# Kernel tuning notes

Hardware: AMD Instinct MI355X
Metric: run time of the kernel (lower is better)

Reference implementation:

```python
import jax, jax.numpy as jnp
import numpy as np

B, S, H, NH, L = 2, 2048, 2048, 16, 512
HD = H // NH  # head_dim = 128


def setup_inputs() -> dict:
    key = jax.random.key(0)
    k1, k2, k3, k4, k5 = jax.random.split(key, 5)
    scale = 0.02  # mimic xavier-scale init
    return {
        "q": jax.random.normal(k1, (B, S, H), dtype=jnp.float32),
        "latent_kv": jax.random.normal(k2, (B, S, L), dtype=jnp.float32),
        "Wq": jax.random.normal(k3, (H, H), dtype=jnp.float32) * scale,
        "Wkv_expand": jax.random.normal(k4, (2 * H, L), dtype=jnp.float32) * scale,
        "Wout": jax.random.normal(k5, (H, H), dtype=jnp.float32) * scale,
    }


def reference(q, latent_kv, Wq, Wkv_expand, Wout):
    b, sq, _ = q.shape
    sk = latent_kv.shape[1]
    # projections (torch Linear: x @ W.T)
    qp = q @ Wq.T                              # [B,Sq,H]
    kv = latent_kv @ Wkv_expand.T              # [B,Sk,2H]
    k, v = jnp.split(kv, 2, axis=-1)           # each [B,Sk,H]
    # split heads -> [B,NH,S,HD]
    qh = qp.reshape(b, sq, NH, HD).transpose(0, 2, 1, 3)
    kh = k.reshape(b, sk, NH, HD).transpose(0, 2, 1, 3)
    vh = v.reshape(b, sk, NH, HD).transpose(0, 2, 1, 3)
    inv_sqrt_d = 1.0 / jnp.sqrt(jnp.float32(HD))
    scores = jnp.einsum("bhqd,bhkd->bhqk", qh, kh) * inv_sqrt_d
    # causal mask (seq_q == seq_k)
    causal = jnp.tril(jnp.ones((sq, sk), dtype=bool))
    scores = jnp.where(causal, scores, jnp.finfo(scores.dtype).min)
    attn = jax.nn.softmax(scores, axis=-1)
    out = jnp.einsum("bhqk,bhkd->bhqd", attn, vh)  # [B,NH,Sq,HD]
    out = out.transpose(0, 2, 1, 3).reshape(b, sq, H)
    return out @ Wout.T
```

## Files before the change

### kernel.cpp

```cpp
#include <hip/hip_runtime.h>

#define SLEN 2048
#define NHEADS 16
#define HDIM 128

typedef __attribute__((ext_vector_type(8))) short bf16x8;
typedef __attribute__((ext_vector_type(4))) float f32x4;
typedef __attribute__((ext_vector_type(16))) float f32x16;

__device__ __forceinline__ unsigned short f2bf(float f) {
  union { float f; unsigned u; } v; v.f = f;
  unsigned r = v.u + 0x7FFFu + ((v.u >> 16) & 1u);
  return (unsigned short)(r >> 16);
}

__device__ __forceinline__ float bf2f(unsigned short h) {
  union { unsigned u; float f; } v; v.u = (unsigned)h << 16;
  return v.f;
}

__device__ __forceinline__ unsigned pkbf(float a, float b) {
  unsigned r;
  asm("v_cvt_pk_bf16_f32 %0, %1, %2" : "=v"(r) : "v"(a), "v"(b));
  return r;
}

__device__ __forceinline__ void gload16(const void* g, void* l) {
  __builtin_amdgcn_global_load_lds(
      (const __attribute__((address_space(1))) unsigned int*)g,
      (__attribute__((address_space(3))) unsigned int*)l, 16, 0, 0);
}

__global__ __launch_bounds__(256) void cvt_all(const float* __restrict__ q,
                                               const float* __restrict__ Wq,
                                               const float* __restrict__ lat,
                                               const float* __restrict__ Wkv,
                                               const float* __restrict__ Wout,
                                               unsigned short* __restrict__ qo,
                                               unsigned short* __restrict__ Wqo,
                                               unsigned short* __restrict__ lato,
                                               unsigned short* __restrict__ Wkvo,
                                               unsigned short* __restrict__ Wouto) {
  const int blk = blockIdx.x;
  const float* in;
  unsigned short* out;
  int base;
  if (blk < 4096)      { in = q;    out = qo;    base = 0; }
  else if (blk < 6144) { in = Wq;   out = Wqo;   base = 4096; }
  else if (blk < 7168) { in = lat;  out = lato;  base = 6144; }
  else if (blk < 8192) { in = Wkv;  out = Wkvo;  base = 7168; }
  else                 { in = Wout; out = Wouto; base = 8192; }
  const int i = (blk - base) * 256 + threadIdx.x;
  const float4* p = reinterpret_cast<const float4*>(in) + (size_t)i * 2;
  float4 a = p[0], b = p[1];
  uint4 o;
  o.x = (unsigned)f2bf(a.x) | ((unsigned)f2bf(a.y) << 16);
  o.y = (unsigned)f2bf(a.z) | ((unsigned)f2bf(a.w) << 16);
  o.z = (unsigned)f2bf(b.x) | ((unsigned)f2bf(b.y) << 16);
  o.w = (unsigned)f2bf(b.z) | ((unsigned)f2bf(b.w) << 16);
  reinterpret_cast<uint4*>(out)[i] = o;
}

template <bool OUT_F32>
__global__ __launch_bounds__(256) void gemm_bt(const unsigned short* __restrict__ A,
                                               const unsigned short* __restrict__ B,
                                               void* __restrict__ Cv,
                                               int M, int N, int K) {
  __shared__ unsigned short As[128 * 32];
  __shared__ unsigned short Bs[128 * 32];
  const int tid = threadIdx.x;
  const int lane = tid & 63, wid = tid >> 6;
  const int g = lane >> 4, q = lane & 15;
  const int nbx = N >> 7;
  const int bx = blockIdx.x % nbx, by = blockIdx.x / nbx;
  const int tM = by << 7, tN = bx << 7;
  const int wm = (wid >> 1) * 64, wn = (wid & 1) * 64;

  f32x4 acc[4][4] = {};

  const int o0 = tid * 16;
  const int r0 = o0 >> 6, c0 = (o0 & 63) >> 1;
  const int r1 = r0 + 64;
  const unsigned short* gA0 = A + (size_t)(tM + r0) * K + c0;
  const unsigned short* gA1 = A + (size_t)(tM + r1) * K + c0;
  const unsigned short* gB0 = B + (size_t)(tN + r0) * K + c0;
  const unsigned short* gB1 = B + (size_t)(tN + r1) * K + c0;
  char* lA = (char*)As;
  char* lB = (char*)Bs;
  const int wo = wid * 1024;

  for (int kt = 0; kt < K; kt += 32) {
    gload16(gA0, lA + wo);
    gload16(gA1, lA + 4096 + wo);
    gload16(gB0, lB + wo);
    gload16(gB1, lB + 4096 + wo);
    gA0 += 32; gA1 += 32; gB0 += 32; gB1 += 32;
    __syncthreads();
    bf16x8 af[4], bfr[4];
#pragma unroll
    for (int i = 0; i < 4; ++i)
      af[i] = *(const bf16x8*)&As[(wm + i * 16 + q) * 32 + g * 8];
#pragma unroll
    for (int j = 0; j < 4; ++j)
      bfr[j] = *(const bf16x8*)&Bs[(wn + j * 16 + q) * 32 + g * 8];
#pragma unroll
    for (int i = 0; i < 4; ++i)
#pragma unroll
      for (int j = 0; j < 4; ++j)
        acc[i][j] = __builtin_amdgcn_mfma_f32_16x16x32_bf16(af[i], bfr[j], acc[i][j], 0, 0, 0);
    __syncthreads();
  }

  if constexpr (OUT_F32) {
    float* C = (float*)Cv;
#pragma unroll
    for (int i = 0; i < 4; ++i)
#pragma unroll
      for (int j = 0; j < 4; ++j)
#pragma unroll
        for (int r = 0; r < 4; ++r)
          C[(size_t)(tM + wm + i * 16 + g * 4 + r) * N + (tN + wn + j * 16 + q)] =
              acc[i][j][r];
  } else {
    unsigned short* C = (unsigned short*)Cv;
#pragma unroll
    for (int i = 0; i < 4; ++i)
#pragma unroll
      for (int j = 0; j < 4; ++j)
#pragma unroll
        for (int r = 0; r < 4; ++r)
          C[(size_t)(tM + wm + i * 16 + g * 4 + r) * N + (tN + wn + j * 16 + q)] =
              f2bf(acc[i][j][r]);
  }
}

__global__ __launch_bounds__(256, 2) void mla_attn(const unsigned short* __restrict__ Q,
                                                   const unsigned short* __restrict__ K,
                                                   const unsigned short* __restrict__ VT,
                                                   unsigned short* __restrict__ Opart,
                                                   float* __restrict__ Stats) {
  __shared__ unsigned short Ks[2][64 * 128];
  __shared__ unsigned short Vs[2][128 * 64];

  const int tid = threadIdx.x, lane = tid & 63, w = tid >> 6;
  const int q5 = lane & 31, half = lane >> 5, q7 = lane & 7;
  const int s = blockIdx.x & 1;
  const int pr = (blockIdx.x >> 1) & 7;
  const int bh = blockIdx.x >> 4;
  const int head = bh & 15, b = bh >> 4;

  const unsigned short* Kbase = K + (size_t)(b * 2048) * 2048 + head * 128;
  const unsigned short* Vbase = VT + (size_t)(b * 2048 + head * 128) * 2048;

  const int r0 = tid >> 4, c0 = tid & 15;
  const unsigned short* kS = Kbase + (size_t)r0 * 2048 + ((c0 ^ r0) << 3);
  const int d0 = tid >> 3, c3 = tid & 7;
  const unsigned short* vS = Vbase + (size_t)d0 * 2048 + ((c3 ^ (d0 & 7)) << 3);

  const float sc_f = 0.08838834764831845f;
  const int arow0 = q5 * 256;
  const int vrow0 = q5 * 128;
  const int q15 = q5 & 15;

  for (int t2 = 0; t2 < 2; ++t2) {
    const int qt = t2 ? pr : 15 - pr;
    const int kt0 = s * (qt + 1);
    const int ktN = kt0 + qt + 1;
    const int myq = qt * 128 + w * 32 + q5;
    const unsigned short* Qrow = Q + (size_t)(b * 2048 + myq) * 2048 + head * 128;

    bf16x8 qf[8];
#pragma unroll
    for (int ks = 0; ks < 8; ++ks)
      qf[ks] = *(const bf16x8*)((const char*)Qrow + ks * 32 + half * 16);

    __syncthreads();

    {
      const int kvb0 = kt0 * 64;
      unsigned short* kd = &Ks[kt0 & 1][0] + tid * 8;
      unsigned short* vd = &Vs[kt0 & 1][0] + tid * 8;
      const unsigned short* ks2 = kS + (size_t)kvb0 * 2048;
      const unsigned short* vs2 = vS + kvb0;
#pragma unroll
      for (int u = 0; u < 4; ++u) {
        gload16(ks2 + (size_t)u * 16 * 2048, kd + u * 2048);
        gload16(vs2 + (size_t)u * 32 * 2048, vd + u * 2048);
      }
    }

    float m2 = -1e30f, l = 0.f;
    f32x16 o[4];
#pragma unroll
    for (int i = 0; i < 16; ++i) { o[0][i] = 0.f; o[1][i] = 0.f; o[2][i] = 0.f; o[3][i] = 0.f; }

    for (int kt = kt0; kt < ktN; ++kt) {
      const int cur = kt & 1;
      asm volatile("s_waitcnt vmcnt(0)" ::: "memory");
      __builtin_amdgcn_s_barrier();

      if (kt + 1 < ktN) {
        const int kvb2 = (kt + 1) * 64;
        unsigned short* kd = &Ks[cur ^ 1][0] + tid * 8;
        unsigned short* vd = &Vs[cur ^ 1][0] + tid * 8;
        const unsigned short* ks2 = kS + (size_t)kvb2 * 2048;
        const unsigned short* vs2 = vS + kvb2;
#pragma unroll
        for (int u = 0; u < 4; ++u) {
          gload16(ks2 + (size_t)u * 16 * 2048, kd + u * 2048);
          gload16(vs2 + (size_t)u * 32 * 2048, vd + u * 2048);
        }
      }

      f32x16 st[2];
#pragma unroll
      for (int i = 0; i < 16; ++i) { st[0][i] = 0.f; st[1][i] = 0.f; }
      const char* kb = (const char*)&Ks[cur][0];
      __builtin_amdgcn_s_setprio(1);
#pragma unroll
      for (int ks = 0; ks < 8; ++ks) {
        const int cd = ks * 2 + half;
#pragma unroll
        for (int m = 0; m < 2; ++m) {
          bf16x8 kf = *(const bf16x8*)(kb + arow0 + m * 8192 + ((cd ^ q15) << 4));
          st[m] = __builtin_amdgcn_mfma_f32_32x32x16_bf16(kf, qf[ks], st[m], 0, 0, 0);
        }
      }
      __builtin_amdgcn_s_setprio(0);

      float t[32];
      const int kvb = kt * 64;
      const bool needmask = (kvb + 63 > qt * 128 + w * 32);
#pragma unroll
      for (int m = 0; m < 2; ++m)
#pragma unroll
        for (int r = 0; r < 16; ++r) {
          float sv = st[m][r] * sc_f;
          if (needmask) {
            const int kvloc = m * 32 + (r & 3) + 8 * (r >> 2) + 4 * half;
            sv = (kvb + kvloc <= myq) ? sv : -3e38f;
          }
          t[m * 16 + r] = sv;
        }
      float mx = t[0];
#pragma unroll
      for (int i = 1; i < 32; ++i) mx = fmaxf(mx, t[i]);
      mx = fmaxf(mx, __shfl_xor(mx, 32));

      if (!__all(mx <= m2 + 8.f)) {
        const float mnew = fmaxf(m2, mx);
        const float rsc = __expf(m2 - mnew);
        m2 = mnew; l *= rsc;
#pragma unroll
        for (int r = 0; r < 16; ++r) {
          const int rowv = (r & 3) + 8 * (r >> 2) + 4 * half;
          const float f = __shfl(rsc, rowv);
          o[0][r] *= f; o[1][r] *= f; o[2][r] *= f; o[3][r] *= f;
        }
      }

      float ts = 0.f;
#pragma unroll
      for (int i = 0; i < 32; ++i) { t[i] = __expf(t[i] - m2); ts += t[i]; }
      ts += __shfl_xor(ts, 32);
      l += ts;

      unsigned wpk[2][4][2];
#pragma unroll
      for (int m = 0; m < 2; ++m)
#pragma unroll
        for (int r4 = 0; r4 < 4; ++r4) {
          wpk[m][r4][0] = pkbf(t[m * 16 + r4 * 4 + 0], t[m * 16 + r4 * 4 + 1]);
          wpk[m][r4][1] = pkbf(t[m * 16 + r4 * 4 + 2], t[m * 16 + r4 * 4 + 3]);
        }

      const char* vb = (const char*)&Vs[cur][0];
#pragma unroll
      for (int ks = 0; ks < 4; ++ks) {
        const int m = ks >> 1, i = ks & 1;
        const unsigned s0 = half ? wpk[m][2 * i][0] : wpk[m][2 * i + 1][0];
        const unsigned s1 = half ? wpk[m][2 * i][1] : wpk[m][2 * i + 1][1];
        const unsigned rv0 = (unsigned)__shfl_xor((int)s0, 32);
        const unsigned rv1 = (unsigned)__shfl_xor((int)s1, 32);
        const unsigned ow0 = half ? wpk[m][2 * i + 1][0] : wpk[m][2 * i][0];
        const unsigned ow1 = half ? wpk[m][2 * i + 1][1] : wpk[m][2 * i][1];
        union { unsigned u[4]; bf16x8 v; } fr;
        fr.u[0] = half ? rv0 : ow0;
        fr.u[1] = half ? rv1 : ow1;
        fr.u[2] = half ? ow0 : rv0;
        fr.u[3] = half ? ow1 : rv1;
        const int cd = ks * 2 + half;
        __builtin_amdgcn_s_setprio(1);
#pragma unroll
        for (int nf = 0; nf < 4; ++nf) {
          bf16x8 vf = *(const bf16x8*)(vb + vrow0 + nf * 4096 + ((cd ^ q7) << 4));
          o[nf] = __builtin_amdgcn_mfma_f32_32x32x16_bf16(fr.v, vf, o[nf], 0, 0, 0);
        }
        __builtin_amdgcn_s_setprio(0);
      }
    }

    const int base_o = ((bh * 16 + qt) * 2 + s) << 14;
    const int base_s = ((bh * 16 + qt) * 2 + s) << 8;
    if (half == 0) {
      Stats[base_s + (w * 32 + q5) * 2] = m2;
      Stats[base_s + (w * 32 + q5) * 2 + 1] = l;
    }
#pragma unroll
    for (int r = 0; r < 16; ++r) {
      const int rowv = (r & 3) + 8 * (r >> 2) + 4 * half;
      const int row = w * 32 + rowv;
#pragma unroll
      for (int nf = 0; nf < 4; ++nf)
        Opart[base_o + row * 128 + nf * 32 + q5] = f2bf(o[nf][r]);
    }
  }
}

__global__ __launch_bounds__(256) void mla_merge(const unsigned short* __restrict__ Op,
                                                 const float* __restrict__ St,
                                                 unsigned short* __restrict__ AO) {
  const int idx = blockIdx.x * 256 + threadIdx.x;
  const int rid = idx >> 4;
  const int d0 = (idx & 15) << 3;
  const int bhqt = rid >> 7;
  const int row = rid & 127;
  const int sb = bhqt << 1;
  const float m1 = St[(sb << 8) + row * 2];
  const float l1 = St[(sb << 8) + row * 2 + 1];
  const float m2 = St[(sb << 8) + 256 + row * 2];
  const float l2 = St[(sb << 8) + 256 + row * 2 + 1];
  const float M = fmaxf(m1, m2);
  const float w1 = __expf(m1 - M), w2 = __expf(m2 - M);
  const float inv = 1.0f / (w1 * l1 + w2 * l2);
  const unsigned short* p1 = Op + ((size_t)sb << 14) + row * 128 + d0;
  bf16x8 a = *(const bf16x8*)p1;
  bf16x8 c = *(const bf16x8*)(p1 + 16384);
  const int bh = bhqt >> 4, qt = bhqt & 15;
  const int head = bh & 15, b = bh >> 4;
  unsigned short outv[8];
#pragma unroll
  for (int j = 0; j < 8; ++j)
    outv[j] = f2bf((w1 * bf2f((unsigned short)a[j]) + w2 * bf2f((unsigned short)c[j])) * inv);
  unsigned short* dst = AO + ((size_t)(b * 2048 + qt * 128 + row)) * 2048 + head * 128 + d0;
  *(uint4*)dst = *(const uint4*)outv;
}

extern "C" void kernel_launch(void* const* d_in, const int* in_sizes, int n_in,
                              void* d_out, int out_size, void* d_ws, size_t ws_size,
                              hipStream_t stream) {
  const float* q    = (const float*)d_in[0];
  const float* lat  = (const float*)d_in[1];
  const float* Wq   = (const float*)d_in[2];
  const float* Wkv  = (const float*)d_in[3];
  const float* Wout = (const float*)d_in[4];

  char* ws = (char*)d_ws;
  unsigned short* qbf   = (unsigned short*)(ws);
  unsigned short* Opart = (unsigned short*)(ws);
  unsigned short* Wqbf  = (unsigned short*)(ws + 16777216);
  unsigned short* latbf = (unsigned short*)(ws + 25165824);
  unsigned short* Wkvbf = (unsigned short*)(ws + 29360128);
  unsigned short* Wobf  = (unsigned short*)(ws + 33554432);
  unsigned short* qpbf  = (unsigned short*)(ws + 41943040);
  unsigned short* Kbf   = (unsigned short*)(ws + 58720256);
  unsigned short* aobf  = (unsigned short*)(ws + 58720256);
  unsigned short* VTbf  = (unsigned short*)(ws + 75497472);
  float*          Stats = (float*)(ws + 92274688);
  unsigned short* Wvbf  = Wkvbf + (size_t)2048 * 512;

  cvt_all<<<10240, 256, 0, stream>>>(q, Wq, lat, Wkv, Wout,
                                     qbf, Wqbf, latbf, Wkvbf, Wobf);

  gemm_bt<false><<<512, 256, 0, stream>>>(qbf, Wqbf, qpbf, 4096, 2048, 2048);
  gemm_bt<false><<<512, 256, 0, stream>>>(latbf, Wkvbf, Kbf, 4096, 2048, 512);
  gemm_bt<false><<<256, 256, 0, stream>>>(Wvbf, latbf, VTbf, 2048, 2048, 512);
  gemm_bt<false><<<256, 256, 0, stream>>>(Wvbf, latbf + (size_t)2048 * 512,
                                          VTbf + (size_t)2048 * 2048, 2048, 2048, 512);
  mla_attn<<<512, 256, 0, stream>>>(qpbf, Kbf, VTbf, Opart, Stats);
  mla_merge<<<4096, 256, 0, stream>>>(Opart, Stats, aobf);
  gemm_bt<true><<<512, 256, 0, stream>>>(aobf, Wobf, (float*)d_out, 4096, 2048, 2048);
}
```

Baseline: 246.7 us.

## Enlarge attention query tile to 256 rows with 8 waves and triple-buffered KV

The attention kernel now runs 512-thread blocks covering 256 query rows, so each K/V tile loaded into shared memory is reused by twice as many waves. K/V staging moves from double to triple buffering with a two-tile prefetch distance and a partial vmcnt wait, so loads overlap more compute. The two V-transpose GEMM launches are merged into one launch using a z-grid batch offset. Costs are higher LDS use (one block per CU) and half as many attention blocks, which may reduce occupancy and worsen causal load balance.

```diff
diff --git a/kernel.cpp b/kernel.cpp
--- a/kernel.cpp
+++ b/kernel.cpp
@@ -65,7 +65,8 @@
 __global__ __launch_bounds__(256) void gemm_bt(const unsigned short* __restrict__ A,
                                                const unsigned short* __restrict__ B,
                                                void* __restrict__ Cv,
-                                               int M, int N, int K) {
+                                               int M, int N, int K,
+                                               size_t zB, size_t zC) {
   __shared__ unsigned short As[128 * 32];
   __shared__ unsigned short Bs[128 * 32];
   const int tid = threadIdx.x;
@@ -75,6 +76,8 @@
   const int bx = blockIdx.x % nbx, by = blockIdx.x / nbx;
   const int tM = by << 7, tN = bx << 7;
   const int wm = (wid >> 1) * 64, wn = (wid & 1) * 64;
+  const size_t zoff = (size_t)blockIdx.z;
+  B += zoff * zB;
 
   f32x4 acc[4][4] = {};
 
@@ -112,7 +115,7 @@
   }
 
   if constexpr (OUT_F32) {
-    float* C = (float*)Cv;
+    float* C = (float*)Cv + zoff * zC;
 #pragma unroll
     for (int i = 0; i < 4; ++i)
 #pragma unroll
@@ -122,7 +125,7 @@
           C[(size_t)(tM + wm + i * 16 + g * 4 + r) * N + (tN + wn + j * 16 + q)] =
               acc[i][j][r];
   } else {
-    unsigned short* C = (unsigned short*)Cv;
+    unsigned short* C = (unsigned short*)Cv + zoff * zC;
 #pragma unroll
     for (int i = 0; i < 4; ++i)
 #pragma unroll
@@ -134,26 +137,26 @@
   }
 }
 
-__global__ __launch_bounds__(256, 2) void mla_attn(const unsigned short* __restrict__ Q,
+__global__ __launch_bounds__(512, 1) void mla_attn(const unsigned short* __restrict__ Q,
                                                    const unsigned short* __restrict__ K,
                                                    const unsigned short* __restrict__ VT,
                                                    unsigned short* __restrict__ Opart,
                                                    float* __restrict__ Stats) {
-  __shared__ unsigned short Ks[2][64 * 128];
-  __shared__ unsigned short Vs[2][128 * 64];
+  __shared__ unsigned short Ks[3][64 * 128];
+  __shared__ unsigned short Vs[3][128 * 64];
 
   const int tid = threadIdx.x, lane = tid & 63, w = tid >> 6;
   const int q5 = lane & 31, half = lane >> 5, q7 = lane & 7;
   const int s = blockIdx.x & 1;
-  const int pr = (blockIdx.x >> 1) & 7;
-  const int bh = blockIdx.x >> 4;
+  const int pr = (blockIdx.x >> 1) & 3;
+  const int bh = blockIdx.x >> 3;
   const int head = bh & 15, b = bh >> 4;
 
   const unsigned short* Kbase = K + (size_t)(b * 2048) * 2048 + head * 128;
   const unsigned short* Vbase = VT + (size_t)(b * 2048 + head * 128) * 2048;
 
   const int r0 = tid >> 4, c0 = tid & 15;
-  const unsigned short* kS = Kbase + (size_t)r0 * 2048 + ((c0 ^ r0) << 3);
+  const unsigned short* kS = Kbase + (size_t)r0 * 2048 + ((c0 ^ (r0 & 15)) << 3);
   const int d0 = tid >> 3, c3 = tid & 7;
   const unsigned short* vS = Vbase + (size_t)d0 * 2048 + ((c3 ^ (d0 & 7)) << 3);
 
@@ -163,10 +166,10 @@
   const int q15 = q5 & 15;
 
   for (int t2 = 0; t2 < 2; ++t2) {
-    const int qt = t2 ? pr : 15 - pr;
-    const int kt0 = s * (qt + 1);
-    const int ktN = kt0 + qt + 1;
-    const int myq = qt * 128 + w * 32 + q5;
+    const int qt = t2 ? pr : 7 - pr;
+    const int kt0 = s * 2 * (qt + 1);
+    const int ktN = kt0 + 2 * (qt + 1);
+    const int myq = qt * 256 + w * 32 + q5;
     const unsigned short* Qrow = Q + (size_t)(b * 2048 + myq) * 2048 + head * 128;
 
     bf16x8 qf[8];
@@ -176,17 +179,26 @@
 
     __syncthreads();
 
+    int cur = kt0 % 3;
     {
+      const int n1 = cur + 1 == 3 ? 0 : cur + 1;
       const int kvb0 = kt0 * 64;
-      unsigned short* kd = &Ks[kt0 & 1][0] + tid * 8;
-      unsigned short* vd = &Vs[kt0 & 1][0] + tid * 8;
+      unsigned short* kd = &Ks[cur][0] + tid * 8;
+      unsigned short* vd = &Vs[cur][0] + tid * 8;
       const unsigned short* ks2 = kS + (size_t)kvb0 * 2048;
       const unsigned short* vs2 = vS + kvb0;
-#pragma unroll
-      for (int u = 0; u < 4; ++u) {
-        gload16(ks2 + (size_t)u * 16 * 2048, kd + u * 2048);
-        gload16(vs2 + (size_t)u * 32 * 2048, vd + u * 2048);
-      }
+      gload16(ks2, kd);
+      gload16(ks2 + (size_t)32 * 2048, kd + 4096);
+      gload16(vs2, vd);
+      gload16(vs2 + (size_t)64 * 2048, vd + 4096);
+      unsigned short* kd1 = &Ks[n1][0] + tid * 8;
+      unsigned short* vd1 = &Vs[n1][0] + tid * 8;
+      const unsigned short* ks3 = ks2 + (size_t)64 * 2048;
+      const unsigned short* vs3 = vs2 + 64;
+      gload16(ks3, kd1);
+      gload16(ks3 + (size_t)32 * 2048, kd1 + 4096);
+      gload16(vs3, vd1);
+      gload16(vs3 + (size_t)64 * 2048, vd1 + 4096);
     }
 
     float m2 = -1e30f, l = 0.f;
@@ -195,21 +207,21 @@
     for (int i = 0; i < 16; ++i) { o[0][i] = 0.f; o[1][i] = 0.f; o[2][i] = 0.f; o[3][i] = 0.f; }
 
     for (int kt = kt0; kt < ktN; ++kt) {
-      const int cur = kt & 1;
-      asm volatile("s_waitcnt vmcnt(0)" ::: "memory");
+      if (kt + 1 < ktN) asm volatile("s_waitcnt vmcnt(4)" ::: "memory");
+      else              asm volatile("s_waitcnt vmcnt(0)" ::: "memory");
       __builtin_amdgcn_s_barrier();
 
-      if (kt + 1 < ktN) {
-        const int kvb2 = (kt + 1) * 64;
-        unsigned short* kd = &Ks[cur ^ 1][0] + tid * 8;
-        unsigned short* vd = &Vs[cur ^ 1][0] + tid * 8;
+      if (kt + 2 < ktN) {
+        const int n2 = cur >= 1 ? cur - 1 : cur + 2;
+        const int kvb2 = (kt + 2) * 64;
+        unsigned short* kd = &Ks[n2][0] + tid * 8;
+        unsigned short* vd = &Vs[n2][0] + tid * 8;
         const unsigned short* ks2 = kS + (size_t)kvb2 * 2048;
         const unsigned short* vs2 = vS + kvb2;
-#pragma unroll
-        for (int u = 0; u < 4; ++u) {
-          gload16(ks2 + (size_t)u * 16 * 2048, kd + u * 2048);
-          gload16(vs2 + (size_t)u * 32 * 2048, vd + u * 2048);
-        }
+        gload16(ks2, kd);
+        gload16(ks2 + (size_t)32 * 2048, kd + 4096);
+        gload16(vs2, vd);
+        gload16(vs2 + (size_t)64 * 2048, vd + 4096);
       }
 
       f32x16 st[2];
@@ -230,7 +242,7 @@
 
       float t[32];
       const int kvb = kt * 64;
-      const bool needmask = (kvb + 63 > qt * 128 + w * 32);
+      const bool needmask = (kvb + 63 > qt * 256 + w * 32);
 #pragma unroll
       for (int m = 0; m < 2; ++m)
 #pragma unroll
@@ -298,10 +310,13 @@
         }
         __builtin_amdgcn_s_setprio(0);
       }
+
+      cur = cur + 1 == 3 ? 0 : cur + 1;
     }
 
-    const int base_o = ((bh * 16 + qt) * 2 + s) << 14;
-    const int base_s = ((bh * 16 + qt) * 2 + s) << 8;
+    const int set = (bh * 8 + qt) * 2 + s;
+    const int base_o = set << 15;
+    const int base_s = set << 9;
     if (half == 0) {
       Stats[base_s + (w * 32 + q5) * 2] = m2;
       Stats[base_s + (w * 32 + q5) * 2 + 1] = l;
@@ -323,26 +338,26 @@
   const int idx = blockIdx.x * 256 + threadIdx.x;
   const int rid = idx >> 4;
   const int d0 = (idx & 15) << 3;
-  const int bhqt = rid >> 7;
-  const int row = rid & 127;
+  const int bhqt = rid >> 8;
+  const int row = rid & 255;
   const int sb = bhqt << 1;
-  const float m1 = St[(sb << 8) + row * 2];
-  const float l1 = St[(sb << 8) + row * 2 + 1];
-  const float m2 = St[(sb << 8) + 256 + row * 2];
-  const float l2 = St[(sb << 8) + 256 + row * 2 + 1];
+  const float m1 = St[(sb << 9) + row * 2];
+  const float l1 = St[(sb << 9) + row * 2 + 1];
+  const float m2 = St[((sb + 1) << 9) + row * 2];
+  const float l2 = St[((sb + 1) << 9) + row * 2 + 1];
   const float M = fmaxf(m1, m2);
   const float w1 = __expf(m1 - M), w2 = __expf(m2 - M);
   const float inv = 1.0f / (w1 * l1 + w2 * l2);
-  const unsigned short* p1 = Op + ((size_t)sb << 14) + row * 128 + d0;
+  const unsigned short* p1 = Op + ((size_t)sb << 15) + row * 128 + d0;
   bf16x8 a = *(const bf16x8*)p1;
-  bf16x8 c = *(const bf16x8*)(p1 + 16384);
-  const int bh = bhqt >> 4, qt = bhqt & 15;
+  bf16x8 c = *(const bf16x8*)(p1 + 32768);
+  const int bh = bhqt >> 3, qt = bhqt & 7;
   const int head = bh & 15, b = bh >> 4;
   unsigned short outv[8];
 #pragma unroll
   for (int j = 0; j < 8; ++j)
     outv[j] = f2bf((w1 * bf2f((unsigned short)a[j]) + w2 * bf2f((unsigned short)c[j])) * inv);
-  unsigned short* dst = AO + ((size_t)(b * 2048 + qt * 128 + row)) * 2048 + head * 128 + d0;
+  unsigned short* dst = AO + ((size_t)(b * 2048 + qt * 256 + row)) * 2048 + head * 128 + d0;
   *(uint4*)dst = *(const uint4*)outv;
 }
 
@@ -372,12 +387,12 @@
   cvt_all<<<10240, 256, 0, stream>>>(q, Wq, lat, Wkv, Wout,
                                      qbf, Wqbf, latbf, Wkvbf, Wobf);
 
-  gemm_bt<false><<<512, 256, 0, stream>>>(qbf, Wqbf, qpbf, 4096, 2048, 2048);
-  gemm_bt<false><<<512, 256, 0, stream>>>(latbf, Wkvbf, Kbf, 4096, 2048, 512);
-  gemm_bt<false><<<256, 256, 0, stream>>>(Wvbf, latbf, VTbf, 2048, 2048, 512);
-  gemm_bt<false><<<256, 256, 0, stream>>>(Wvbf, latbf + (size_t)2048 * 512,
-                                          VTbf + (size_t)2048 * 2048, 2048, 2048, 512);
-  mla_attn<<<512, 256, 0, stream>>>(qpbf, Kbf, VTbf, Opart, Stats);
+  gemm_bt<false><<<512, 256, 0, stream>>>(qbf, Wqbf, qpbf, 4096, 2048, 2048, 0, 0);
+  gemm_bt<false><<<512, 256, 0, stream>>>(latbf, Wkvbf, Kbf, 4096, 2048, 512, 0, 0);
+  gemm_bt<false><<<dim3(256, 1, 2), 256, 0, stream>>>(
+      Wvbf, latbf, VTbf, 2048, 2048, 512,
+      (size_t)2048 * 512, (size_t)2048 * 2048);
+  mla_attn<<<256, 512, 0, stream>>>(qpbf, Kbf, VTbf, Opart, Stats);
   mla_merge<<<4096, 256, 0, stream>>>(Opart, Stats, aobf);
-  gemm_bt<true><<<512, 256, 0, stream>>>(aobf, Wobf, (float*)d_out, 4096, 2048, 2048);
-}
+  gemm_bt<true><<<512, 256, 0, stream>>>(aobf, Wobf, (float*)d_out, 4096, 2048, 2048, 0, 0);
+}
```

Result: faster. 240.7 us (-2.4%).

## Fold softmax scale into Q projection, split K/V waits, batch V GEMMs

Applied to the files above, without the earlier changes.

Multiplies the Q projection output by 1/sqrt(d)·log2(e) so the attention loop drops its per-score multiply and uses exp2 directly. The merge kernel and the skip-rescale threshold are adjusted to match the base-2 domain. K loads are issued before V loads, and a partial vmcnt wait plus a second barrier let the V tile keep arriving while the QK^T and softmax work runs. The two V-transpose GEMM launches are merged into one launch with a z-dimension. Storing pre-scaled Q in bf16 slightly changes rounding, and the extra barrier adds some synchronisation cost.

```diff
diff --git a/kernel.cpp b/kernel.cpp
--- a/kernel.cpp
+++ b/kernel.cpp
@@ -65,7 +65,8 @@
 __global__ __launch_bounds__(256) void gemm_bt(const unsigned short* __restrict__ A,
                                                const unsigned short* __restrict__ B,
                                                void* __restrict__ Cv,
-                                               int M, int N, int K) {
+                                               int M, int N, int K,
+                                               size_t zB, size_t zC, float scale) {
   __shared__ unsigned short As[128 * 32];
   __shared__ unsigned short Bs[128 * 32];
   const int tid = threadIdx.x;
@@ -75,6 +76,8 @@
   const int bx = blockIdx.x % nbx, by = blockIdx.x / nbx;
   const int tM = by << 7, tN = bx << 7;
   const int wm = (wid >> 1) * 64, wn = (wid & 1) * 64;
+  const size_t zoff = (size_t)blockIdx.z;
+  B += zoff * zB;
 
   f32x4 acc[4][4] = {};
 
@@ -112,7 +115,7 @@
   }
 
   if constexpr (OUT_F32) {
-    float* C = (float*)Cv;
+    float* C = (float*)Cv + zoff * zC;
 #pragma unroll
     for (int i = 0; i < 4; ++i)
 #pragma unroll
@@ -120,9 +123,9 @@
 #pragma unroll
         for (int r = 0; r < 4; ++r)
           C[(size_t)(tM + wm + i * 16 + g * 4 + r) * N + (tN + wn + j * 16 + q)] =
-              acc[i][j][r];
+              acc[i][j][r] * scale;
   } else {
-    unsigned short* C = (unsigned short*)Cv;
+    unsigned short* C = (unsigned short*)Cv + zoff * zC;
 #pragma unroll
     for (int i = 0; i < 4; ++i)
 #pragma unroll
@@ -130,7 +133,7 @@
 #pragma unroll
         for (int r = 0; r < 4; ++r)
           C[(size_t)(tM + wm + i * 16 + g * 4 + r) * N + (tN + wn + j * 16 + q)] =
-              f2bf(acc[i][j][r]);
+              f2bf(acc[i][j][r] * scale);
   }
 }
 
@@ -157,7 +160,6 @@
   const int d0 = tid >> 3, c3 = tid & 7;
   const unsigned short* vS = Vbase + (size_t)d0 * 2048 + ((c3 ^ (d0 & 7)) << 3);
 
-  const float sc_f = 0.08838834764831845f;
   const int arow0 = q5 * 256;
   const int vrow0 = q5 * 128;
   const int q15 = q5 & 15;
@@ -183,10 +185,9 @@
       const unsigned short* ks2 = kS + (size_t)kvb0 * 2048;
       const unsigned short* vs2 = vS + kvb0;
 #pragma unroll
-      for (int u = 0; u < 4; ++u) {
-        gload16(ks2 + (size_t)u * 16 * 2048, kd + u * 2048);
-        gload16(vs2 + (size_t)u * 32 * 2048, vd + u * 2048);
-      }
+      for (int u = 0; u < 4; ++u) gload16(ks2 + (size_t)u * 16 * 2048, kd + u * 2048);
+#pragma unroll
+      for (int u = 0; u < 4; ++u) gload16(vs2 + (size_t)u * 32 * 2048, vd + u * 2048);
     }
 
     float m2 = -1e30f, l = 0.f;
@@ -196,7 +197,7 @@
 
     for (int kt = kt0; kt < ktN; ++kt) {
       const int cur = kt & 1;
-      asm volatile("s_waitcnt vmcnt(0)" ::: "memory");
+      asm volatile("s_waitcnt vmcnt(4)" ::: "memory");
       __builtin_amdgcn_s_barrier();
 
       if (kt + 1 < ktN) {
@@ -206,10 +207,9 @@
         const unsigned short* ks2 = kS + (size_t)kvb2 * 2048;
         const unsigned short* vs2 = vS + kvb2;
 #pragma unroll
-        for (int u = 0; u < 4; ++u) {
-          gload16(ks2 + (size_t)u * 16 * 2048, kd + u * 2048);
-          gload16(vs2 + (size_t)u * 32 * 2048, vd + u * 2048);
-        }
+        for (int u = 0; u < 4; ++u) gload16(ks2 + (size_t)u * 16 * 2048, kd + u * 2048);
+#pragma unroll
+        for (int u = 0; u < 4; ++u) gload16(vs2 + (size_t)u * 32 * 2048, vd + u * 2048);
       }
 
       f32x16 st[2];
@@ -235,21 +235,21 @@
       for (int m = 0; m < 2; ++m)
 #pragma unroll
         for (int r = 0; r < 16; ++r) {
-          float sv = st[m][r] * sc_f;
+          float sv = st[m][r];
           if (needmask) {
             const int kvloc = m * 32 + (r & 3) + 8 * (r >> 2) + 4 * half;
             sv = (kvb + kvloc <= myq) ? sv : -3e38f;
           }
           t[m * 16 + r] = sv;
         }
-      float mx = t[0];
-#pragma unroll
-      for (int i = 1; i < 32; ++i) mx = fmaxf(mx, t[i]);
+      float mx = fmaxf(t[0], t[1]);
+#pragma unroll
+      for (int i = 2; i < 32; i += 2) mx = fmaxf(fmaxf(mx, t[i]), t[i + 1]);
       mx = fmaxf(mx, __shfl_xor(mx, 32));
 
-      if (!__all(mx <= m2 + 8.f)) {
+      if (!__all(mx <= m2 + 11.54f)) {
         const float mnew = fmaxf(m2, mx);
-        const float rsc = __expf(m2 - mnew);
+        const float rsc = __builtin_amdgcn_exp2f(m2 - mnew);
         m2 = mnew; l *= rsc;
 #pragma unroll
         for (int r = 0; r < 16; ++r) {
@@ -261,7 +261,7 @@
 
       float ts = 0.f;
 #pragma unroll
-      for (int i = 0; i < 32; ++i) { t[i] = __expf(t[i] - m2); ts += t[i]; }
+      for (int i = 0; i < 32; ++i) { t[i] = __builtin_amdgcn_exp2f(t[i] - m2); ts += t[i]; }
       ts += __shfl_xor(ts, 32);
       l += ts;
 
@@ -273,6 +273,10 @@
           wpk[m][r4][0] = pkbf(t[m * 16 + r4 * 4 + 0], t[m * 16 + r4 * 4 + 1]);
           wpk[m][r4][1] = pkbf(t[m * 16 + r4 * 4 + 2], t[m * 16 + r4 * 4 + 3]);
         }
+
+      if (kt + 1 < ktN) asm volatile("s_waitcnt vmcnt(8)" ::: "memory");
+      else              asm volatile("s_waitcnt vmcnt(0)" ::: "memory");
+      __builtin_amdgcn_s_barrier();
 
       const char* vb = (const char*)&Vs[cur][0];
 #pragma unroll
@@ -300,8 +304,9 @@
       }
     }
 
-    const int base_o = ((bh * 16 + qt) * 2 + s) << 14;
-    const int base_s = ((bh * 16 + qt) * 2 + s) << 8;
+    const int set = (bh * 16 + qt) * 2 + s;
+    const int base_o = set << 14;
+    const int base_s = set << 8;
     if (half == 0) {
       Stats[base_s + (w * 32 + q5) * 2] = m2;
       Stats[base_s + (w * 32 + q5) * 2 + 1] = l;
@@ -331,7 +336,8 @@
   const float m2 = St[(sb << 8) + 256 + row * 2];
   const float l2 = St[(sb << 8) + 256 + row * 2 + 1];
   const float M = fmaxf(m1, m2);
-  const float w1 = __expf(m1 - M), w2 = __expf(m2 - M);
+  const float w1 = __builtin_amdgcn_exp2f(m1 - M);
+  const float w2 = __builtin_amdgcn_exp2f(m2 - M);
   const float inv = 1.0f / (w1 * l1 + w2 * l2);
   const unsigned short* p1 = Op + ((size_t)sb << 14) + row * 128 + d0;
   bf16x8 a = *(const bf16x8*)p1;
@@ -369,15 +375,17 @@
   float*          Stats = (float*)(ws + 92274688);
   unsigned short* Wvbf  = Wkvbf + (size_t)2048 * 512;
 
+  const float SCALE_L2E = 0.12751742f;
+
   cvt_all<<<10240, 256, 0, stream>>>(q, Wq, lat, Wkv, Wout,
                                      qbf, Wqbf, latbf, Wkvbf, Wobf);
 
-  gemm_bt<false><<<512, 256, 0, stream>>>(qbf, Wqbf, qpbf, 4096, 2048, 2048);
-  gemm_bt<false><<<512, 256, 0, stream>>>(latbf, Wkvbf, Kbf, 4096, 2048, 512);
-  gemm_bt<false><<<256, 256, 0, stream>>>(Wvbf, latbf, VTbf, 2048, 2048, 512);
-  gemm_bt<false><<<256, 256, 0, stream>>>(Wvbf, latbf + (size_t)2048 * 512,
-                                          VTbf + (size_t)2048 * 2048, 2048, 2048, 512);
+  gemm_bt<false><<<512, 256, 0, stream>>>(qbf, Wqbf, qpbf, 4096, 2048, 2048, 0, 0, SCALE_L2E);
+  gemm_bt<false><<<512, 256, 0, stream>>>(latbf, Wkvbf, Kbf, 4096, 2048, 512, 0, 0, 1.0f);
+  gemm_bt<false><<<dim3(256, 1, 2), 256, 0, stream>>>(
+      Wvbf, latbf, VTbf, 2048, 2048, 512,
+      (size_t)2048 * 512, (size_t)2048 * 2048, 1.0f);
   mla_attn<<<512, 256, 0, stream>>>(qpbf, Kbf, VTbf, Opart, Stats);
   mla_merge<<<4096, 256, 0, stream>>>(Opart, Stats, aobf);
-  gemm_bt<true><<<512, 256, 0, stream>>>(aobf, Wobf, (float*)d_out, 4096, 2048, 2048);
-}
+  gemm_bt<true><<<512, 256, 0, stream>>>(aobf, Wobf, (float*)d_out, 4096, 2048, 2048, 0, 0, 1.0f);
+}
```

Result: faster. 234.3 us (-5.0%).
